# Kernel tuning notes

Measured on AMD Instinct MI355X. Metric: run time of the kernel, lower is better.

Reference implementation:

```python
import jax, jax.numpy as jnp
import numpy as np

DIM = 256
NUM_HEADS = 8
HEAD_DIM = DIM // NUM_HEADS
WH, WW = 7, 7
N = WH * WW              # tokens per window = 49
NUM_WINDOWS = 64         # windows per image (56x56 map / 7x7 windows)
B_TOTAL = 2048           # num_windows * B_images
SCALE = HEAD_DIM ** -0.5


def _relative_position_index():
    # Matches the tf.meshgrid (xy indexing) construction in the source.
    coords = np.stack(np.meshgrid(np.arange(WH), np.arange(WW)), axis=0)  # [2, WW, WH]
    flat = coords.reshape(2, -1)                                          # [2, N]
    rel = flat[:, :, None] - flat[:, None, :]                             # [2, N, N]
    rel = rel.transpose(1, 2, 0).astype(np.int32)                         # [N, N, 2]
    rel[:, :, 0] += WH - 1
    rel[:, :, 1] += WW - 1
    rel[:, :, 0] *= 2 * WW - 1
    return rel.sum(-1)                                                    # [N, N]


def setup_inputs() -> dict:
    key = jax.random.key(0)
    ks = jax.random.split(key, 6)
    std = 0.02
    x = jax.random.normal(ks[0], (B_TOTAL, N, DIM), dtype=jnp.float32)
    mask = jnp.zeros((NUM_WINDOWS, N, N), dtype=jnp.float32)  # 0 / -inf additive mask
    qkv_w = jax.random.normal(ks[1], (DIM, 3 * DIM), dtype=jnp.float32) * std
    qkv_b = jnp.zeros((3 * DIM,), dtype=jnp.float32)
    proj_w = jax.random.normal(ks[2], (DIM, DIM), dtype=jnp.float32) * std
    proj_b = jnp.zeros((DIM,), dtype=jnp.float32)
    n_rel = (2 * WH - 1) * (2 * WW - 1)  # 169
    bias_table = jax.random.normal(ks[3], (n_rel, NUM_HEADS), dtype=jnp.float32) * std
    rel_index = jnp.asarray(_relative_position_index(), dtype=jnp.int32)
    return {"x": x, "mask": mask, "qkv_w": qkv_w, "qkv_b": qkv_b,
            "proj_w": proj_w, "proj_b": proj_b, "bias_table": bias_table,
            "rel_index": rel_index}


def reference(x, mask, qkv_w, qkv_b, proj_w, proj_b, bias_table, rel_index):
    B = x.shape[0]
    # qkv projection -> [3, B, H, N, hd]
    qkv = x @ qkv_w + qkv_b                                  # [B, N, 3C]
    qkv = qkv.reshape(B, N, 3, NUM_HEADS, HEAD_DIM)
    qkv = jnp.transpose(qkv, (2, 0, 3, 1, 4))
    q, k, v = qkv[0], qkv[1], qkv[2]
    # scaled attention scores [B, H, N, N]
    attn = jnp.einsum('bhnd,bhmd->bhnm', q, k) * SCALE
    # relative position bias gather: [N*N] -> [N, N, H] -> [1, H, N, N]
    bias = bias_table[rel_index.reshape(-1)].reshape(N, N, NUM_HEADS)
    attn = attn + jnp.transpose(bias, (2, 0, 1))[None]
    # additive window mask [nW, N, N]
    nW = mask.shape[0]
    attn = attn.reshape(B // nW, nW, NUM_HEADS, N, N) + mask[None, :, None]
    attn = attn.reshape(B, NUM_HEADS, N, N)
    attn = jax.nn.softmax(attn, axis=-1)
    out = jnp.einsum('bhnm,bhmd->bhnd', attn, v)             # [B, H, N, hd]
    out = jnp.transpose(out, (0, 2, 1, 3)).reshape(B, N, DIM)
    return out @ proj_w + proj_b
```

## Files before the change

### kernel.cpp

```cpp
#include <hip/hip_runtime.h>

#define NTOK 49
#define NHEAD 8
#define HDIM 32
#define DIMC 256
#define SCALE_F 0.17677669529663687f

typedef __attribute__((ext_vector_type(8))) short short8;
typedef __attribute__((ext_vector_type(4))) float f32x4;

#define AS1P(p) ((__attribute__((address_space(1))) void*)(p))
#define AS3P(p) ((__attribute__((address_space(3))) void*)(p))

__device__ inline unsigned short f2bf(float f) {
    unsigned int u = __float_as_uint(f);
    u += 0x7fffu + ((u >> 16) & 1u);
    return (unsigned short)(u >> 16);
}

__global__ __launch_bounds__(256) void conv_bf16(const float* __restrict__ in,
    unsigned short* __restrict__ outp, int nv8)
{
    int i = blockIdx.x * 256 + threadIdx.x;
    if (i >= nv8) return;
    const float4* p = (const float4*)in + (size_t)i * 2;
    float4 a = p[0], b = p[1];
    union { unsigned short s[8]; uint4 v; } u;
    u.s[0] = f2bf(a.x); u.s[1] = f2bf(a.y); u.s[2] = f2bf(a.z); u.s[3] = f2bf(a.w);
    u.s[4] = f2bf(b.x); u.s[5] = f2bf(b.y); u.s[6] = f2bf(b.z); u.s[7] = f2bf(b.w);
    ((uint4*)outp)[i] = u.v;
}

__global__ __launch_bounds__(256) void pack_w(const float* __restrict__ W,
    unsigned short* __restrict__ Wp, int K, int N)
{
    int idx = blockIdx.x * 256 + threadIdx.x;
    if (idx >= K * N) return;
    int k = idx / N, n = idx - k * N;
    Wp[((size_t)(k >> 3) * N + n) * 8 + (k & 7)] = f2bf(W[idx]);
}

__global__ __launch_bounds__(256) void bm_build(const float* __restrict__ bias_table,
    const int* __restrict__ rel_index, const float* __restrict__ mask,
    float* __restrict__ bm)
{
    int idx = blockIdx.x * 256 + threadIdx.x;
    if (idx >= 64 * NHEAD * NTOK * NTOK) return;
    int wh = idx / (NTOK * NTOK);
    int ij = idx - wh * (NTOK * NTOK);
    int w = wh >> 3, h = wh & 7;
    bm[idx] = bias_table[rel_index[ij] * NHEAD + h] + mask[(size_t)w * (NTOK * NTOK) + ij];
}

template <bool OUT_BF16>
__global__ __launch_bounds__(256) void gemm_mfma(
    const unsigned short* __restrict__ A,
    const unsigned short* __restrict__ Wp,
    const float* __restrict__ Bv,
    void* __restrict__ Yv,
    int N)
{
    __shared__ __align__(16) unsigned short As[4096];
    __shared__ __align__(16) unsigned short Bs[4096];

    const int tid  = threadIdx.x;
    const int lane = tid & 63;
    const int wv   = tid >> 6;
    const int quad = lane >> 4;
    const int l15  = lane & 15;
    const long m0  = (long)blockIdx.y * 128;
    const int  n0  = blockIdx.x * 128;
    const int  wm  = (wv >> 1) * 64;
    const int  wn  = (wv & 1) * 64;

    const unsigned short* ga0 = A + (size_t)(m0 + lane) * 256 + wv * 8;
    const unsigned short* ga1 = A + (size_t)(m0 + 64 + lane) * 256 + wv * 8;
    const unsigned short* gb0 = Wp + ((size_t)wv * N + n0 + lane) * 8;
    const unsigned short* gb1 = Wp + ((size_t)wv * N + n0 + 64 + lane) * 8;

    f32x4 acc[4][4];
    #pragma unroll
    for (int i = 0; i < 4; ++i)
        #pragma unroll
        for (int j = 0; j < 4; ++j) acc[i][j] = (f32x4){0.f, 0.f, 0.f, 0.f};

    for (int k0 = 0; k0 < 256; k0 += 32) {
        const size_t bofs = (size_t)(k0 >> 3) * N * 8;
        __builtin_amdgcn_global_load_lds(AS1P(ga0 + k0),   AS3P(As + wv * 1024),       16, 0, 0);
        __builtin_amdgcn_global_load_lds(AS1P(ga1 + k0),   AS3P(As + wv * 1024 + 512), 16, 0, 0);
        __builtin_amdgcn_global_load_lds(AS1P(gb0 + bofs), AS3P(Bs + wv * 1024),       16, 0, 0);
        __builtin_amdgcn_global_load_lds(AS1P(gb1 + bofs), AS3P(Bs + wv * 1024 + 512), 16, 0, 0);
        __syncthreads();
        short8 af[4], bq[4];
        #pragma unroll
        for (int t = 0; t < 4; ++t) {
            af[t] = *(const short8*)(As + quad * 1024 + (wm + t * 16 + l15) * 8);
            bq[t] = *(const short8*)(Bs + quad * 1024 + (wn + t * 16 + l15) * 8);
        }
        #pragma unroll
        for (int ti = 0; ti < 4; ++ti)
            #pragma unroll
            for (int tj = 0; tj < 4; ++tj)
                acc[ti][tj] = __builtin_amdgcn_mfma_f32_16x16x32_bf16(af[ti], bq[tj], acc[ti][tj], 0, 0, 0);
        __syncthreads();
    }

    #pragma unroll
    for (int ti = 0; ti < 4; ++ti) {
        #pragma unroll
        for (int r = 0; r < 4; ++r) {
            const long row = m0 + wm + ti * 16 + quad * 4 + r;
            #pragma unroll
            for (int tj = 0; tj < 4; ++tj) {
                const int col = n0 + wn + tj * 16 + l15;
                float v = acc[ti][tj][r] + Bv[col];
                if (OUT_BF16) ((unsigned short*)Yv)[row * N + col] = f2bf(v);
                else          ((float*)Yv)[row * N + col] = v;
            }
        }
    }
}

__global__ __launch_bounds__(64) void attn_mfma(
    const unsigned short* __restrict__ qkvb,
    const float* __restrict__ bm,
    unsigned short* __restrict__ o1b,
    int win0)
{
    __shared__ __align__(16) unsigned short Qs[2048];
    __shared__ __align__(16) unsigned short Ks[2048];
    __shared__ __align__(16) unsigned short Ps[4096];
    __shared__ __align__(16) unsigned short Vt[2304];

    const int lane = threadIdx.x;
    const int b    = blockIdx.x;
    const int h    = blockIdx.y;
    const int w    = (win0 + b) & 63;
    const int quad = lane >> 4;
    const int l15  = lane & 15;

    uint4 qw[4], kw[4], vw[4];
    const unsigned short* rp = qkvb + ((size_t)b * NTOK + lane) * 768 + h * HDIM;
    if (lane < NTOK) {
        #pragma unroll
        for (int c = 0; c < 4; ++c) {
            qw[c] = *(const uint4*)(rp + c * 8);
            kw[c] = *(const uint4*)(rp + 256 + c * 8);
            vw[c] = *(const uint4*)(rp + 512 + c * 8);
        }
    } else {
        #pragma unroll
        for (int c = 0; c < 4; ++c) {
            qw[c] = make_uint4(0u, 0u, 0u, 0u); kw[c] = qw[c]; vw[c] = qw[c];
        }
    }
    #pragma unroll
    for (int c = 0; c < 4; ++c) {
        *(uint4*)(Qs + c * 512 + lane * 8) = qw[c];
        *(uint4*)(Ks + c * 512 + lane * 8) = kw[c];
    }
    #pragma unroll
    for (int c = 0; c < 4; ++c) {
        unsigned int uu[4] = {vw[c].x, vw[c].y, vw[c].z, vw[c].w};
        #pragma unroll
        for (int e = 0; e < 4; ++e) {
            int d = c * 8 + e * 2;
            Vt[(size_t)d * 72 + lane]       = (unsigned short)(uu[e] & 0xffffu);
            Vt[(size_t)(d + 1) * 72 + lane] = (unsigned short)(uu[e] >> 16);
        }
    }
    __syncthreads();

    short8 aq[4], bk[4];
    #pragma unroll
    for (int t = 0; t < 4; ++t) {
        aq[t] = *(const short8*)(Qs + quad * 512 + (t * 16 + l15) * 8);
        bk[t] = *(const short8*)(Ks + quad * 512 + (t * 16 + l15) * 8);
    }
    f32x4 sa[4][4];
    #pragma unroll
    for (int ti = 0; ti < 4; ++ti)
        #pragma unroll
        for (int tj = 0; tj < 4; ++tj) {
            f32x4 z = (f32x4){0.f, 0.f, 0.f, 0.f};
            sa[ti][tj] = __builtin_amdgcn_mfma_f32_16x16x32_bf16(aq[ti], bk[tj], z, 0, 0, 0);
        }

    const float* bmb = bm + (size_t)(w * NHEAD + h) * (NTOK * NTOK);
    float inv[4][4];
    #pragma unroll
    for (int ti = 0; ti < 4; ++ti) {
        #pragma unroll
        for (int r = 0; r < 4; ++r) {
            const int row = ti * 16 + quad * 4 + r;
            float sv[4];
            #pragma unroll
            for (int tj = 0; tj < 4; ++tj) {
                const int col = tj * 16 + l15;
                float s;
                if (col < NTOK) {
                    float add = (row < NTOK) ? bmb[row * NTOK + col] : 0.f;
                    s = sa[ti][tj][r] * SCALE_F + add;
                } else {
                    s = -__builtin_inff();
                }
                sv[tj] = s;
            }
            float mx = fmaxf(fmaxf(sv[0], sv[1]), fmaxf(sv[2], sv[3]));
            mx = fmaxf(mx, __shfl_xor(mx, 1, 16));
            mx = fmaxf(mx, __shfl_xor(mx, 2, 16));
            mx = fmaxf(mx, __shfl_xor(mx, 4, 16));
            mx = fmaxf(mx, __shfl_xor(mx, 8, 16));
            float e0 = __expf(sv[0] - mx), e1 = __expf(sv[1] - mx);
            float e2 = __expf(sv[2] - mx), e3 = __expf(sv[3] - mx);
            sa[ti][0][r] = e0; sa[ti][1][r] = e1; sa[ti][2][r] = e2; sa[ti][3][r] = e3;
            float sum = (e0 + e1) + (e2 + e3);
            sum += __shfl_xor(sum, 1, 16);
            sum += __shfl_xor(sum, 2, 16);
            sum += __shfl_xor(sum, 4, 16);
            sum += __shfl_xor(sum, 8, 16);
            inv[ti][r] = 1.f / sum;
        }
    }

    #pragma unroll
    for (int ti = 0; ti < 4; ++ti)
        #pragma unroll
        for (int tj = 0; tj < 4; ++tj)
            #pragma unroll
            for (int r = 0; r < 4; ++r) {
                const int row = ti * 16 + quad * 4 + r;
                const int col = tj * 16 + l15;
                Ps[((col >> 3) * 64 + row) * 8 + (col & 7)] = f2bf(sa[ti][tj][r]);
            }
    __syncthreads();

    short8 pa[4][2], vb2[2][2];
    #pragma unroll
    for (int ti = 0; ti < 4; ++ti)
        #pragma unroll
        for (int kc = 0; kc < 2; ++kc)
            pa[ti][kc] = *(const short8*)(Ps + ((kc * 4 + quad) * 64 + ti * 16 + l15) * 8);
    #pragma unroll
    for (int td = 0; td < 2; ++td)
        #pragma unroll
        for (int kc = 0; kc < 2; ++kc)
            vb2[td][kc] = *(const short8*)(Vt + (size_t)(td * 16 + l15) * 72 + (kc * 4 + quad) * 8);
    f32x4 oa[4][2];
    #pragma unroll
    for (int ti = 0; ti < 4; ++ti)
        #pragma unroll
        for (int td = 0; td < 2; ++td) {
            f32x4 z = (f32x4){0.f, 0.f, 0.f, 0.f};
            z = __builtin_amdgcn_mfma_f32_16x16x32_bf16(pa[ti][0], vb2[td][0], z, 0, 0, 0);
            oa[ti][td] = __builtin_amdgcn_mfma_f32_16x16x32_bf16(pa[ti][1], vb2[td][1], z, 0, 0, 0);
        }

    #pragma unroll
    for (int ti = 0; ti < 4; ++ti)
        #pragma unroll
        for (int r = 0; r < 4; ++r) {
            const int row = ti * 16 + quad * 4 + r;
            if (row < NTOK) {
                const float si = inv[ti][r];
                unsigned short* op = o1b + ((size_t)b * NTOK + row) * DIMC + h * HDIM;
                #pragma unroll
                for (int td = 0; td < 2; ++td)
                    op[td * 16 + l15] = f2bf(oa[ti][td][r] * si);
            }
        }
}

extern "C" void kernel_launch(void* const* d_in, const int* in_sizes, int n_in,
                              void* d_out, int out_size, void* d_ws, size_t ws_size,
                              hipStream_t stream)
{
    const float* x          = (const float*)d_in[0];
    const float* mask       = (const float*)d_in[1];
    const float* qkv_w      = (const float*)d_in[2];
    const float* qkv_b      = (const float*)d_in[3];
    const float* proj_w     = (const float*)d_in[4];
    const float* proj_b     = (const float*)d_in[5];
    const float* bias_table = (const float*)d_in[6];
    const int*   rel_index  = (const int*)d_in[7];
    float* outp = (float*)d_out;

    const int B_TOTAL = 2048;
    char* ws = (char*)d_ws;
    size_t off = 0;
    auto carve = [&](size_t bytes) -> void* {
        void* p = ws + off; off += (bytes + 255) & ~(size_t)255; return p;
    };
    unsigned short* WpQ = (unsigned short*)carve((size_t)256 * 768 * 2);
    unsigned short* WpP = (unsigned short*)carve((size_t)256 * 256 * 2);
    float* bm = (float*)carve((size_t)64 * NHEAD * NTOK * NTOK * 4);
    const size_t fixed = off;
    const size_t PER_WIN = (size_t)NTOK * 256 * 2 + (size_t)NTOK * 768 * 2 + (size_t)NTOK * 256 * 2;
    size_t avail = (ws_size > fixed + 1024) ? (ws_size - fixed - 1024) : 0;
    int chunkW = (int)(avail / PER_WIN);
    if (chunkW > B_TOTAL) chunkW = B_TOTAL;
    chunkW &= ~127;
    if (chunkW < 128) chunkW = 128;
    unsigned short* x_bf = (unsigned short*)carve((size_t)chunkW * NTOK * 256 * 2);
    unsigned short* qkvb = (unsigned short*)carve((size_t)chunkW * NTOK * 768 * 2);
    unsigned short* o1b  = (unsigned short*)carve((size_t)chunkW * NTOK * 256 * 2);

    pack_w<<<(256 * 768 + 255) / 256, 256, 0, stream>>>(qkv_w, WpQ, 256, 768);
    pack_w<<<(256 * 256 + 255) / 256, 256, 0, stream>>>(proj_w, WpP, 256, 256);
    bm_build<<<(64 * NHEAD * NTOK * NTOK + 255) / 256, 256, 0, stream>>>(
        bias_table, rel_index, mask, bm);

    for (int w0 = 0; w0 < B_TOTAL; w0 += chunkW) {
        int wc = B_TOTAL - w0; if (wc > chunkW) wc = chunkW;
        const int Mc = wc * NTOK;
        const int nv8 = Mc * 32;
        conv_bf16<<<(nv8 + 255) / 256, 256, 0, stream>>>(
            x + (size_t)w0 * NTOK * DIMC, x_bf, nv8);
        gemm_mfma<true ><<<dim3(6, Mc / 128), 256, 0, stream>>>(x_bf, WpQ, qkv_b, qkvb, 768);
        attn_mfma<<<dim3(wc, NHEAD), 64, 0, stream>>>(qkvb, bm, o1b, w0);
        gemm_mfma<false><<<dim3(2, Mc / 128), 256, 0, stream>>>(
            o1b, WpP, proj_b, outp + (size_t)w0 * NTOK * DIMC, 256);
    }
}
```

Baseline: 465.5 us.

## Load Q/K fragments directly from global and alias V/P LDS per wave

The attention kernel now loads Q and K MFMA operand fragments straight from global memory instead of staging them in shared memory. The transposed V tile and the probability tile share one per-wave LDS buffer, with a barrier placed before P overwrites V. Each block now runs two heads of the same window as two waves. The aim is to cut LDS footprint and traffic, drop a staging barrier, and raise occupancy. In exchange the global loads are less coalesced and padded rows rely on clamped reads.

Result: faster. 400.5 us (-14.0%).

```diff
diff --git a/kernel.cpp b/kernel.cpp
--- a/kernel.cpp
+++ b/kernel.cpp
@@ -121,62 +121,52 @@
     }
 }
 
-__global__ __launch_bounds__(64) void attn_mfma(
+__global__ __launch_bounds__(128) void attn_mfma(
     const unsigned short* __restrict__ qkvb,
     const float* __restrict__ bm,
     unsigned short* __restrict__ o1b,
     int win0)
 {
-    __shared__ __align__(16) unsigned short Qs[2048];
-    __shared__ __align__(16) unsigned short Ks[2048];
-    __shared__ __align__(16) unsigned short Ps[4096];
-    __shared__ __align__(16) unsigned short Vt[2304];
-
-    const int lane = threadIdx.x;
-    const int b    = blockIdx.x;
-    const int h    = blockIdx.y;
+    __shared__ __align__(16) unsigned short SMEM[2 * 3528];
+
+    const int wvid = threadIdx.x >> 6;
+    const int lane = threadIdx.x & 63;
+    const int h    = blockIdx.x * 2 + wvid;
+    const int b    = blockIdx.y;
     const int w    = (win0 + b) & 63;
     const int quad = lane >> 4;
     const int l15  = lane & 15;
 
-    uint4 qw[4], kw[4], vw[4];
-    const unsigned short* rp = qkvb + ((size_t)b * NTOK + lane) * 768 + h * HDIM;
-    if (lane < NTOK) {
+    unsigned short* Vt = SMEM + wvid * 3528;
+    unsigned short* Ps = SMEM + wvid * 3528;
+
+    const unsigned short* wbase = qkvb + (size_t)b * NTOK * 768 + h * HDIM;
+
+    {
+        const int tok = (lane < NTOK) ? lane : (NTOK - 1);
+        const unsigned short* vp = wbase + (size_t)tok * 768 + 512;
         #pragma unroll
         for (int c = 0; c < 4; ++c) {
-            qw[c] = *(const uint4*)(rp + c * 8);
-            kw[c] = *(const uint4*)(rp + 256 + c * 8);
-            vw[c] = *(const uint4*)(rp + 512 + c * 8);
-        }
-    } else {
-        #pragma unroll
-        for (int c = 0; c < 4; ++c) {
-            qw[c] = make_uint4(0u, 0u, 0u, 0u); kw[c] = qw[c]; vw[c] = qw[c];
-        }
-    }
-    #pragma unroll
-    for (int c = 0; c < 4; ++c) {
-        *(uint4*)(Qs + c * 512 + lane * 8) = qw[c];
-        *(uint4*)(Ks + c * 512 + lane * 8) = kw[c];
-    }
-    #pragma unroll
-    for (int c = 0; c < 4; ++c) {
-        unsigned int uu[4] = {vw[c].x, vw[c].y, vw[c].z, vw[c].w};
-        #pragma unroll
-        for (int e = 0; e < 4; ++e) {
-            int d = c * 8 + e * 2;
-            Vt[(size_t)d * 72 + lane]       = (unsigned short)(uu[e] & 0xffffu);
-            Vt[(size_t)(d + 1) * 72 + lane] = (unsigned short)(uu[e] >> 16);
-        }
-    }
-    __syncthreads();
+            uint4 vv = *(const uint4*)(vp + c * 8);
+            unsigned int uu[4] = {vv.x, vv.y, vv.z, vv.w};
+            #pragma unroll
+            for (int e = 0; e < 4; ++e) {
+                int d = c * 8 + e * 2;
+                Vt[d * 72 + lane]       = (unsigned short)(uu[e] & 0xffffu);
+                Vt[(d + 1) * 72 + lane] = (unsigned short)(uu[e] >> 16);
+            }
+        }
+    }
 
     short8 aq[4], bk[4];
     #pragma unroll
     for (int t = 0; t < 4; ++t) {
-        aq[t] = *(const short8*)(Qs + quad * 512 + (t * 16 + l15) * 8);
-        bk[t] = *(const short8*)(Ks + quad * 512 + (t * 16 + l15) * 8);
-    }
+        int row = t * 16 + l15; if (row >= NTOK) row = NTOK - 1;
+        const unsigned short* rp = wbase + (size_t)row * 768 + quad * 8;
+        aq[t] = *(const short8*)(rp);
+        bk[t] = *(const short8*)(rp + 256);
+    }
+
     f32x4 sa[4][4];
     #pragma unroll
     for (int ti = 0; ti < 4; ++ti)
@@ -185,6 +175,13 @@
             f32x4 z = (f32x4){0.f, 0.f, 0.f, 0.f};
             sa[ti][tj] = __builtin_amdgcn_mfma_f32_16x16x32_bf16(aq[ti], bk[tj], z, 0, 0, 0);
         }
+
+    short8 vb2[2][2];
+    #pragma unroll
+    for (int td = 0; td < 2; ++td)
+        #pragma unroll
+        for (int kc = 0; kc < 2; ++kc)
+            vb2[td][kc] = *(const short8*)(Vt + (td * 16 + l15) * 72 + kc * 32 + quad * 8);
 
     const float* bmb = bm + (size_t)(w * NHEAD + h) * (NTOK * NTOK);
     float inv[4][4];
@@ -223,29 +220,28 @@
         }
     }
 
+    __syncthreads();
+
     #pragma unroll
     for (int ti = 0; ti < 4; ++ti)
         #pragma unroll
-        for (int tj = 0; tj < 4; ++tj)
-            #pragma unroll
-            for (int r = 0; r < 4; ++r) {
-                const int row = ti * 16 + quad * 4 + r;
-                const int col = tj * 16 + l15;
-                Ps[((col >> 3) * 64 + row) * 8 + (col & 7)] = f2bf(sa[ti][tj][r]);
-            }
-    __syncthreads();
-
-    short8 pa[4][2], vb2[2][2];
-    #pragma unroll
-    for (int ti = 0; ti < 4; ++ti)
+        for (int r = 0; r < 4; ++r) {
+            const int row = ti * 16 + quad * 4 + r;
+            if (row < NTOK) {
+                #pragma unroll
+                for (int tj = 0; tj < 4; ++tj)
+                    Ps[row * 72 + tj * 16 + l15] = f2bf(sa[ti][tj][r]);
+            }
+        }
+
+    short8 pa[4][2];
+    #pragma unroll
+    for (int ti = 0; ti < 4; ++ti) {
+        int row = ti * 16 + l15; if (row >= NTOK) row = NTOK - 1;
         #pragma unroll
         for (int kc = 0; kc < 2; ++kc)
-            pa[ti][kc] = *(const short8*)(Ps + ((kc * 4 + quad) * 64 + ti * 16 + l15) * 8);
-    #pragma unroll
-    for (int td = 0; td < 2; ++td)
-        #pragma unroll
-        for (int kc = 0; kc < 2; ++kc)
-            vb2[td][kc] = *(const short8*)(Vt + (size_t)(td * 16 + l15) * 72 + (kc * 4 + quad) * 8);
+            pa[ti][kc] = *(const short8*)(Ps + row * 72 + kc * 32 + quad * 8);
+    }
     f32x4 oa[4][2];
     #pragma unroll
     for (int ti = 0; ti < 4; ++ti)
@@ -317,7 +313,7 @@
         conv_bf16<<<(nv8 + 255) / 256, 256, 0, stream>>>(
             x + (size_t)w0 * NTOK * DIMC, x_bf, nv8);
         gemm_mfma<true ><<<dim3(6, Mc / 128), 256, 0, stream>>>(x_bf, WpQ, qkv_b, qkvb, 768);
-        attn_mfma<<<dim3(wc, NHEAD), 64, 0, stream>>>(qkvb, bm, o1b, w0);
+        attn_mfma<<<dim3(NHEAD / 2, wc), 128, 0, stream>>>(qkvb, bm, o1b, w0);
         gemm_mfma<false><<<dim3(2, Mc / 128), 256, 0, stream>>>(
             o1b, WpP, proj_b, outp + (size_t)w0 * NTOK * DIMC, 256);
     }
```
